# Performance work log

Measured on AMD Instinct MI355X. Metric: run time of the kernel, lower is better.

## Reference

```python
import jax, jax.numpy as jnp
import numpy as np
from jax import lax

C = 256      # in_c == out_c == dim
NH = 8       # num_heads
K = 7        # depthwise pos-enc kernel
H1 = 512     # int(mlp_ratio * in_c) = 2.0 * 256
B, Hs, Ws = 2, 48, 48


def setup_inputs() -> dict:
    key = jax.random.key(0)
    ks = jax.random.split(key, 8)
    w = lambda k, shape: jax.random.normal(k, shape, jnp.float32) * 0.02
    return {
        "x": jax.random.normal(ks[0], (B, C, Hs, Ws), jnp.float32),
        # 1x1 convs stored as [out, in] (BN folded into weight+bias)
        "qk_w": w(ks[1], (2 * C, C)), "qk_b": jnp.zeros((2 * C,), jnp.float32),
        "v_w": w(ks[2], (C, C)),       "v_b": jnp.zeros((C,), jnp.float32),
        # depthwise positional encoding conv [C,1,K,K]
        "pe_w": w(ks[3], (C, 1, K, K)), "pe_b": jnp.zeros((C,), jnp.float32),
        "proj_w": w(ks[4], (C, C)),    "proj_b": jnp.zeros((C,), jnp.float32),
        # conv FFN: 1x1 (SiLU) -> 1x1 (no act)
        "fc1_w": w(ks[5], (H1, C)),    "fc1_b": jnp.zeros((H1,), jnp.float32),
        "fc2_w": w(ks[6], (C, H1)),    "fc2_b": jnp.zeros((C,), jnp.float32),
    }


def _c1(x, w, b):
    # 1x1 conv == per-pixel matmul
    return jnp.einsum('bchw,oc->bohw', x, w) + b[None, :, None, None]


def reference(x, qk_w, qk_b, v_w, v_b, pe_w, pe_b, proj_w, proj_b,
              fc1_w, fc1_b, fc2_w, fc2_b):
    Bb, Cc, Hh, Ww = x.shape
    hd = Cc // NH                 # head_dim = 32
    N = Hh * Ww
    scale = hd ** -0.5

    # ---- AttentionV2 ----
    qk = _c1(x, qk_w, qk_b).reshape(Bb, NH, 2 * hd, N)
    q, k = qk[:, :, :hd], qk[:, :, hd:]
    v_full = _c1(x, v_w, v_b)                      # [B,C,H,W]
    pe = lax.conv_general_dilated(
        v_full, pe_w, (1, 1), 'SAME', feature_group_count=Cc,
        dimension_numbers=('NCHW', 'OIHW', 'NCHW')) + pe_b[None, :, None, None]
    v = v_full.reshape(Bb, NH, hd, N)

    # attn = q^T @ k * scale ; softmax over keys
    attn = jax.nn.softmax(jnp.einsum('bhdn,bhdm->bhnm', q, k) * scale, axis=-1)
    o = jnp.einsum('bhdm,bhnm->bhdn', v, attn).reshape(Bb, Cc, Hh, Ww)
    attn_out = _c1(o + pe, proj_w, proj_b)

    # ---- block residuals + conv FFN (add=True) ----
    x1 = x + attn_out
    h = jax.nn.silu(_c1(x1, fc1_w, fc1_b))         # Conv(in_c, hidden, 1, 1) with SiLU
    return x1 + _c1(h, fc2_w, fc2_b)               # Conv(hidden, out_c, 1, act=False)
```

## Files before the change

kernel.cpp:

```cpp
#include <hip/hip_runtime.h>
#include <hip/hip_bf16.h>

#define NCH 256
#define NHD 8
#define HD 32
#define NPIX 2304
#define H1DIM 512

typedef __attribute__((ext_vector_type(8))) __bf16 bf16x8;
typedef __attribute__((ext_vector_type(4))) float f32x4;

__global__ __launch_bounds__(256) void wcast_k(
    const float* __restrict__ w0, const float* __restrict__ w1,
    const float* __restrict__ w2, const float* __restrict__ w3,
    const float* __restrict__ w4, __bf16* __restrict__ dst) {
    int i = blockIdx.x * 256 + threadIdx.x;
    const float* src; int off;
    if (i < 32768)      { src = w0; off = i; }
    else if (i < 49152) { src = w1; off = i - 32768; }
    else if (i < 65536) { src = w2; off = i - 49152; }
    else if (i < 98304) { src = w3; off = i - 65536; }
    else                { src = w4; off = i - 98304; }
    float4 v = ((const float4*)src)[off];
    union { __bf16 h[4]; uint2 u; } pk;
    pk.h[0] = (__bf16)v.x; pk.h[1] = (__bf16)v.y;
    pk.h[2] = (__bf16)v.z; pk.h[3] = (__bf16)v.w;
    ((uint2*)dst)[i] = pk.u;
}

__global__ __launch_bounds__(256) void nchw2nhwc_k(const float* __restrict__ s1,
                                                   __bf16* __restrict__ dst) {
    const int tid = threadIdx.x;
    const int n0 = blockIdx.x * 64;
    const int c0 = blockIdx.y * 64;
    const int b = blockIdx.z;
    __shared__ float tile[64][65];
    const size_t sb = ((size_t)b * NCH + c0) * NPIX + n0;
#pragma unroll
    for (int i = 0; i < 16; ++i) {
        int idx = tid + i * 256;
        int r = idx >> 6, c = idx & 63;
        tile[r][c] = s1[sb + (size_t)r * NPIX + c];
    }
    __syncthreads();
#pragma unroll
    for (int i = 0; i < 8; ++i) {
        int idx = tid + i * 256;
        int nn = idx >> 5, cp = (idx & 31) * 2;
        union { __bf16 h[2]; unsigned u; } pk;
        pk.h[0] = (__bf16)tile[cp][nn];
        pk.h[1] = (__bf16)tile[cp + 1][nn];
        *(unsigned*)&dst[((size_t)b * NPIX + n0 + nn) * NCH + c0 + cp] = pk.u;
    }
}

template <int IC, int OC, int MODE>
__global__ __launch_bounds__(64) void convmm_k(
    const __bf16* __restrict__ A, const __bf16* __restrict__ W,
    const float* __restrict__ bias, const float* __restrict__ resid,
    float* __restrict__ out_f, __bf16* __restrict__ out_b,
    __bf16* __restrict__ out_b2) {
    const int lane = threadIdx.x;
    const int l16 = lane & 15, quad = lane >> 4;
    const int m0 = blockIdx.x * 16;
    const int oc0 = blockIdx.y * 16;
    const int b = blockIdx.z;

    const __bf16* aptr = A + ((size_t)b * NPIX + m0 + l16) * IC + quad * 8;
    const __bf16* bptr = W + (size_t)(oc0 + l16) * IC + quad * 8;

    f32x4 acc = {0.f, 0.f, 0.f, 0.f};
#pragma unroll 8
    for (int k = 0; k < IC; k += 32) {
        bf16x8 af = *(const bf16x8*)(aptr + k);
        bf16x8 bf = *(const bf16x8*)(bptr + k);
        acc = __builtin_amdgcn_mfma_f32_16x16x32_bf16(af, bf, acc, 0, 0, 0);
    }

    const int oc = oc0 + l16;
    const int mb = m0 + quad * 4;
    const float bb = bias[oc];

    if constexpr (MODE == 0) {
        const int h = oc0 >> 6;
        const int bh = b * NHD + h;
        const int dd = (oc0 & 16) + l16;
        if ((oc0 & 32) == 0) {
            const float qs = 0.17677669529663689f * 1.4426950408889634f;
#pragma unroll
            for (int r = 0; r < 4; ++r)
                out_b[((size_t)bh * NPIX + mb + r) * 32 + dd] = (__bf16)((acc[r] + bb) * qs);
        } else {
            __bf16* kp = out_b2 + ((size_t)(bh * 144 + (m0 >> 4)) * 64 + (dd >> 3) * 16 + quad * 4) * 8 + (dd & 7);
#pragma unroll
            for (int r = 0; r < 4; ++r) kp[r * 8] = (__bf16)(acc[r] + bb);
        }
    } else if constexpr (MODE == 1) {
        const int h = oc0 >> 5;
        const int bh = b * NHD + h;
        const int half = (oc0 >> 4) & 1;
        const size_t fb = ((size_t)b * OC + oc) * NPIX + mb;
        float4 vf_; float* vp = &vf_.x;
        union { __bf16 hh[4]; uint2 u; } pk;
#pragma unroll
        for (int r = 0; r < 4; ++r) {
            float v = acc[r] + bb;
            vp[r] = v; pk.hh[r] = (__bf16)v;
        }
        *(float4*)&out_f[fb] = vf_;
        *(uint2*)&out_b[((size_t)(bh * 144 + (m0 >> 4)) * 64 + lane) * 8 + half * 4] = pk.u;
    } else if constexpr (MODE == 2) {
        const size_t fb = ((size_t)b * OC + oc) * NPIX + mb;
        float4 xr = *(const float4*)&resid[fb];
        const float* xp = &xr.x;
        float4 vf_; float* vp = &vf_.x;
#pragma unroll
        for (int r = 0; r < 4; ++r) {
            float v = acc[r] + bb + xp[r];
            vp[r] = v;
            out_b[((size_t)b * NPIX + mb + r) * OC + oc] = (__bf16)v;
        }
        *(float4*)&out_f[fb] = vf_;
    } else if constexpr (MODE == 3) {
#pragma unroll
        for (int r = 0; r < 4; ++r) {
            float v = acc[r] + bb;
            v = v / (1.f + __expf(-v));
            out_b[((size_t)b * NPIX + mb + r) * OC + oc] = (__bf16)v;
        }
    } else {
        const size_t fb = ((size_t)b * OC + oc) * NPIX + mb;
        float4 xr = *(const float4*)&resid[fb];
        const float* xp = &xr.x;
        float4 vf_; float* vp = &vf_.x;
#pragma unroll
        for (int r = 0; r < 4; ++r) vp[r] = acc[r] + bb + xp[r];
        *(float4*)&out_f[fb] = vf_;
    }
}

__global__ __launch_bounds__(256) void dwconv_k(const float* __restrict__ vb,
                                                const float* __restrict__ pw,
                                                const float* __restrict__ pb,
                                                float* __restrict__ pe) {
    const int c = blockIdx.x, b = blockIdx.y, tid = threadIdx.x;
    __shared__ float plane[NPIX];
    __shared__ float wk[49];
    const size_t base = ((size_t)b * NCH + c) * NPIX;
    for (int i = tid; i < NPIX; i += 256) plane[i] = vb[base + i];
    if (tid < 49) wk[tid] = pw[c * 49 + tid];
    float bb = pb[c];
    __syncthreads();
    for (int p = tid; p < NPIX; p += 256) {
        int y = p / 48, x = p - y * 48;
        float s = bb;
#pragma unroll
        for (int ky = 0; ky < 7; ++ky) {
            int yy = y + ky - 3;
            if ((unsigned)yy < 48u) {
#pragma unroll
                for (int kx = 0; kx < 7; ++kx) {
                    int xx = x + kx - 3;
                    if ((unsigned)xx < 48u) s += wk[ky * 7 + kx] * plane[yy * 48 + xx];
                }
            }
        }
        pe[base + p] = s;
    }
}

__global__ __launch_bounds__(256) void attn_mfma4_k(const __bf16* __restrict__ Qb,
                                                    const __bf16* __restrict__ Kf,
                                                    const __bf16* __restrict__ Vf,
                                                    float* __restrict__ opart,
                                                    float* __restrict__ lpart) {
    const int tid = threadIdx.x;
    const int wave = tid >> 6, lane = tid & 63;
    const int l16 = lane & 15, quad = lane >> 4;
    const int nb = blockIdx.x * 128;
    const int h = blockIdx.y;
    const int b = blockIdx.z >> 2, ks = blockIdx.z & 3;
    const int bh = b * NHD + h;
    const int qb = nb + wave * 32;

    bf16x8 b_q0 = *(const bf16x8*)(Qb + ((size_t)bh * NPIX + qb + l16) * 32 + quad * 8);
    bf16x8 b_q1 = *(const bf16x8*)(Qb + ((size_t)bh * NPIX + qb + 16 + l16) * 32 + quad * 8);

    const __bf16* kf = Kf + ((size_t)(bh * 144 + ks * 36) * 64 + lane) * 8;
    const __bf16* vf = Vf + ((size_t)(bh * 144 + ks * 36) * 64 + lane) * 8;

    f32x4 o00 = {0.f,0.f,0.f,0.f}, o01 = {0.f,0.f,0.f,0.f};
    f32x4 o10 = {0.f,0.f,0.f,0.f}, o11 = {0.f,0.f,0.f,0.f};
    f32x4 l0 = {0.f,0.f,0.f,0.f}, l1 = {0.f,0.f,0.f,0.f};

#pragma unroll 3
    for (int t = 0; t < 36; ++t) {
        bf16x8 a_k = *(const bf16x8*)(kf + (size_t)t * 512);
        bf16x8 va  = *(const bf16x8*)(vf + (size_t)t * 512);
        f32x4 z = {0.f, 0.f, 0.f, 0.f};
        f32x4 s0 = __builtin_amdgcn_mfma_f32_16x16x32_bf16(a_k, b_q0, z, 0, 0, 0);
        f32x4 s1 = __builtin_amdgcn_mfma_f32_16x16x32_bf16(a_k, b_q1, z, 0, 0, 0);
        f32x4 p0, p1;
#pragma unroll
        for (int r = 0; r < 4; ++r) {
            p0[r] = __builtin_amdgcn_exp2f(s0[r]);
            p1[r] = __builtin_amdgcn_exp2f(s1[r]);
        }
        l0 += p0; l1 += p1;
        bf16x8 b0lo = {}, b0hi = {}, b1lo = {}, b1hi = {};
#pragma unroll
        for (int r = 0; r < 4; ++r) {
            __bf16 c0 = (__bf16)p0[r], c1 = (__bf16)p1[r];
            b0lo[r] = c0; b0hi[4 + r] = c0;
            b1lo[r] = c1; b1hi[4 + r] = c1;
        }
        o00 = __builtin_amdgcn_mfma_f32_16x16x32_bf16(va, b0lo, o00, 0, 0, 0);
        o01 = __builtin_amdgcn_mfma_f32_16x16x32_bf16(va, b0hi, o01, 0, 0, 0);
        o10 = __builtin_amdgcn_mfma_f32_16x16x32_bf16(va, b1lo, o10, 0, 0, 0);
        o11 = __builtin_amdgcn_mfma_f32_16x16x32_bf16(va, b1hi, o11, 0, 0, 0);
    }

    float ls0 = l0[0] + l0[1] + l0[2] + l0[3];
    ls0 += __shfl_xor(ls0, 16); ls0 += __shfl_xor(ls0, 32);
    float ls1 = l1[0] + l1[1] + l1[2] + l1[3];
    ls1 += __shfl_xor(ls1, 16); ls1 += __shfl_xor(ls1, 32);

    float* op = opart + (size_t)(ks * 16 + bh) * 32 * NPIX;
    const int n0 = qb + l16, n1 = qb + 16 + l16;
#pragma unroll
    for (int r = 0; r < 4; ++r) {
        op[(size_t)(quad * 4 + r) * NPIX + n0]      = o00[r];
        op[(size_t)(16 + quad * 4 + r) * NPIX + n0] = o01[r];
        op[(size_t)(quad * 4 + r) * NPIX + n1]      = o10[r];
        op[(size_t)(16 + quad * 4 + r) * NPIX + n1] = o11[r];
    }
    if (quad == 0) {
        lpart[(size_t)(ks * 16 + bh) * NPIX + n0] = ls0;
        lpart[(size_t)(ks * 16 + bh) * NPIX + n1] = ls1;
    }
}

__global__ __launch_bounds__(256) void merge2_k(const float* __restrict__ opart,
                                                const float* __restrict__ lpart,
                                                const float* __restrict__ pe,
                                                __bf16* __restrict__ opb) {
    const int tid = threadIdx.x;
    const int n0 = blockIdx.x * 64;
    const int h = blockIdx.y, b = blockIdx.z;
    const int bh = b * NHD + h;

    __shared__ float tinv[64];
    __shared__ float tile[64][33];

    if (tid < 64) {
        const int n = n0 + tid;
        float l = 0.f;
#pragma unroll
        for (int s = 0; s < 4; ++s) l += lpart[(size_t)(s * 16 + bh) * NPIX + n];
        tinv[tid] = 1.f / l;
    }
    __syncthreads();

#pragma unroll
    for (int pass = 0; pass < 8; ++pass) {
        const int idx = pass * 256 + tid;
        const int d = idx >> 6, c = idx & 63;
        float v = 0.f;
#pragma unroll
        for (int s = 0; s < 4; ++s)
            v += opart[((size_t)(s * 16 + bh) * 32 + d) * NPIX + n0 + c];
        v = v * tinv[c] + pe[((size_t)(b * NCH + h * HD + d)) * NPIX + n0 + c];
        tile[c][d] = v;
    }
    __syncthreads();

    const int n = tid >> 2, j = tid & 3;
    union { __bf16 hh[8]; uint4 u; } pk;
#pragma unroll
    for (int e = 0; e < 8; ++e) pk.hh[e] = (__bf16)tile[n][j * 8 + e];
    *(uint4*)&opb[((size_t)(b * NPIX + n0 + n)) * NCH + h * HD + j * 8] = pk.u;
}

extern "C" void kernel_launch(void* const* d_in, const int* in_sizes, int n_in,
                              void* d_out, int out_size, void* d_ws, size_t ws_size,
                              hipStream_t stream) {
    const float* x    = (const float*)d_in[0];
    const float* qk_w = (const float*)d_in[1];
    const float* qk_b = (const float*)d_in[2];
    const float* v_w  = (const float*)d_in[3];
    const float* v_b  = (const float*)d_in[4];
    const float* pe_w = (const float*)d_in[5];
    const float* pe_b = (const float*)d_in[6];
    const float* pj_w = (const float*)d_in[7];
    const float* pj_b = (const float*)d_in[8];
    const float* f1_w = (const float*)d_in[9];
    const float* f1_b = (const float*)d_in[10];
    const float* f2_w = (const float*)d_in[11];
    const float* f2_b = (const float*)d_in[12];
    float* out = (float*)d_out;

    const int B = 2;
    const size_t plane = (size_t)NCH * NPIX;
    const size_t bp = (size_t)B * plane;

    float* v_bu  = (float*)d_ws;
    float* pe_bu = v_bu + bp;
    float* x1_f  = pe_bu + bp;
    float* opart = x1_f + bp;
    float* lpart = opart + 4 * bp;
    __bf16* Xb   = (__bf16*)(lpart + 147456);
    __bf16* opb  = Xb + bp;
    __bf16* x1b  = opb + bp;
    __bf16* hb   = x1b + bp;
    __bf16* Qb   = hb + 2 * bp;
    __bf16* Kf   = Qb + bp;
    __bf16* Vf   = Kf + bp;
    __bf16* Wall = Vf + bp;
    __bf16* Wq = Wall;
    __bf16* Wv = Wall + 131072;
    __bf16* Wp = Wall + 196608;
    __bf16* W1 = Wall + 262144;
    __bf16* W2 = Wall + 393216;

    wcast_k<<<512, 256, 0, stream>>>(qk_w, v_w, pj_w, f1_w, f2_w, Wall);
    nchw2nhwc_k<<<dim3(NPIX / 64, 4, B), 256, 0, stream>>>(x, Xb);
    convmm_k<256, 512, 0><<<dim3(NPIX / 16, 32, B), 64, 0, stream>>>(
        Xb, Wq, qk_b, nullptr, nullptr, Qb, Kf);
    convmm_k<256, 256, 1><<<dim3(NPIX / 16, 16, B), 64, 0, stream>>>(
        Xb, Wv, v_b, nullptr, v_bu, Vf, nullptr);
    dwconv_k<<<dim3(NCH, B), 256, 0, stream>>>(v_bu, pe_w, pe_b, pe_bu);
    attn_mfma4_k<<<dim3(NPIX / 128, NHD, B * 4), 256, 0, stream>>>(Qb, Kf, Vf, opart, lpart);
    merge2_k<<<dim3(NPIX / 64, NHD, B), 256, 0, stream>>>(opart, lpart, pe_bu, opb);
    convmm_k<256, 256, 2><<<dim3(NPIX / 16, 16, B), 64, 0, stream>>>(
        opb, Wp, pj_b, x, x1_f, x1b, nullptr);
    convmm_k<256, 512, 3><<<dim3(NPIX / 16, 32, B), 64, 0, stream>>>(
        x1b, W1, f1_b, nullptr, nullptr, hb, nullptr);
    convmm_k<512, 256, 4><<<dim3(NPIX / 16, 16, B), 64, 0, stream>>>(
        hb, W2, f2_b, x1_f, out, nullptr, nullptr);
}
```

Baseline: 219.9 us.

## Fuse prep kernels, merge QK/V projections, drop attention split-K and merge pass

Combines the weight cast and NCHW-to-NHWC transpose into one launch, fuses the QK and V 1x1 projections into a single kernel, and removes the 4-way key split in attention so each wave normalizes and adds the positional encoding directly, eliminating the fp32 partial buffers and the merge kernel. The conv matmuls now pack four waves per block. Fewer launches and less intermediate traffic are the aim, but attention now runs 1152 single-wave blocks each iterating over all 144 key tiles, which reduces parallelism and lengthens the serial loop. Output stores become scattered 2-byte writes.

```diff
diff --git a/kernel.cpp b/kernel.cpp
--- a/kernel.cpp
+++ b/kernel.cpp
@@ -10,59 +10,122 @@
 typedef __attribute__((ext_vector_type(8))) __bf16 bf16x8;
 typedef __attribute__((ext_vector_type(4))) float f32x4;
 
-__global__ __launch_bounds__(256) void wcast_k(
+__global__ __launch_bounds__(256) void prep_k(
+    const float* __restrict__ x,
     const float* __restrict__ w0, const float* __restrict__ w1,
     const float* __restrict__ w2, const float* __restrict__ w3,
-    const float* __restrict__ w4, __bf16* __restrict__ dst) {
-    int i = blockIdx.x * 256 + threadIdx.x;
-    const float* src; int off;
-    if (i < 32768)      { src = w0; off = i; }
-    else if (i < 49152) { src = w1; off = i - 32768; }
-    else if (i < 65536) { src = w2; off = i - 49152; }
-    else if (i < 98304) { src = w3; off = i - 65536; }
-    else                { src = w4; off = i - 98304; }
-    float4 v = ((const float4*)src)[off];
-    union { __bf16 h[4]; uint2 u; } pk;
-    pk.h[0] = (__bf16)v.x; pk.h[1] = (__bf16)v.y;
-    pk.h[2] = (__bf16)v.z; pk.h[3] = (__bf16)v.w;
-    ((uint2*)dst)[i] = pk.u;
-}
-
-__global__ __launch_bounds__(256) void nchw2nhwc_k(const float* __restrict__ s1,
-                                                   __bf16* __restrict__ dst) {
+    const float* __restrict__ w4,
+    __bf16* __restrict__ Xb, __bf16* __restrict__ Wall) {
     const int tid = threadIdx.x;
-    const int n0 = blockIdx.x * 64;
-    const int c0 = blockIdx.y * 64;
+    if (blockIdx.x < 288) {
+        const int t = blockIdx.x;
+        const int b = t / 144, r0 = t % 144;
+        const int c0 = (r0 / 36) * 64, n0 = (r0 % 36) * 64;
+        __shared__ float tile[64][65];
+        const size_t sb = ((size_t)b * NCH + c0) * NPIX + n0;
+#pragma unroll
+        for (int i = 0; i < 16; ++i) {
+            int idx = tid + i * 256;
+            int rr = idx >> 6, cc = idx & 63;
+            tile[rr][cc] = x[sb + (size_t)rr * NPIX + cc];
+        }
+        __syncthreads();
+#pragma unroll
+        for (int i = 0; i < 8; ++i) {
+            int idx = tid + i * 256;
+            int nn = idx >> 5, cp = (idx & 31) * 2;
+            union { __bf16 h[2]; unsigned u; } pk;
+            pk.h[0] = (__bf16)tile[cp][nn];
+            pk.h[1] = (__bf16)tile[cp + 1][nn];
+            *(unsigned*)&Xb[((size_t)b * NPIX + n0 + nn) * NCH + c0 + cp] = pk.u;
+        }
+    } else {
+        int i = (blockIdx.x - 288) * 256 + tid;
+        const float* src; int off;
+        if (i < 32768)      { src = w0; off = i; }
+        else if (i < 49152) { src = w1; off = i - 32768; }
+        else if (i < 65536) { src = w2; off = i - 49152; }
+        else if (i < 98304) { src = w3; off = i - 65536; }
+        else                { src = w4; off = i - 98304; }
+        float4 v = ((const float4*)src)[off];
+        union { __bf16 h[4]; uint2 u; } pk;
+        pk.h[0] = (__bf16)v.x; pk.h[1] = (__bf16)v.y;
+        pk.h[2] = (__bf16)v.z; pk.h[3] = (__bf16)v.w;
+        ((uint2*)Wall)[i] = pk.u;
+    }
+}
+
+__global__ __launch_bounds__(256) void qkv_k(
+    const __bf16* __restrict__ A, const __bf16* __restrict__ Wq,
+    const __bf16* __restrict__ Wv, const float* __restrict__ qk_b,
+    const float* __restrict__ v_b, __bf16* __restrict__ Qb,
+    __bf16* __restrict__ Kf, float* __restrict__ v_bu,
+    __bf16* __restrict__ Vf) {
+    const int tid = threadIdx.x;
+    const int wave = tid >> 6, lane = tid & 63;
+    const int l16 = lane & 15, quad = lane >> 4;
+    const int m0 = blockIdx.x * 64 + wave * 16;
     const int b = blockIdx.z;
-    __shared__ float tile[64][65];
-    const size_t sb = ((size_t)b * NCH + c0) * NPIX + n0;
-#pragma unroll
-    for (int i = 0; i < 16; ++i) {
-        int idx = tid + i * 256;
-        int r = idx >> 6, c = idx & 63;
-        tile[r][c] = s1[sb + (size_t)r * NPIX + c];
-    }
-    __syncthreads();
-#pragma unroll
-    for (int i = 0; i < 8; ++i) {
-        int idx = tid + i * 256;
-        int nn = idx >> 5, cp = (idx & 31) * 2;
-        union { __bf16 h[2]; unsigned u; } pk;
-        pk.h[0] = (__bf16)tile[cp][nn];
-        pk.h[1] = (__bf16)tile[cp + 1][nn];
-        *(unsigned*)&dst[((size_t)b * NPIX + n0 + nn) * NCH + c0 + cp] = pk.u;
+    const bool isv = blockIdx.y >= 32;
+    const int oc0 = (isv ? (blockIdx.y - 32) : blockIdx.y) * 16;
+    const __bf16* W = isv ? Wv : Wq;
+
+    const __bf16* aptr = A + ((size_t)b * NPIX + m0 + l16) * NCH + quad * 8;
+    const __bf16* bptr = W + (size_t)(oc0 + l16) * NCH + quad * 8;
+
+    f32x4 acc = {0.f, 0.f, 0.f, 0.f};
+#pragma unroll 8
+    for (int k = 0; k < NCH; k += 32) {
+        bf16x8 af = *(const bf16x8*)(aptr + k);
+        bf16x8 bf = *(const bf16x8*)(bptr + k);
+        acc = __builtin_amdgcn_mfma_f32_16x16x32_bf16(af, bf, acc, 0, 0, 0);
+    }
+
+    const int oc = oc0 + l16;
+    const int mb = m0 + quad * 4;
+
+    if (!isv) {
+        const float bb = qk_b[oc];
+        const int h = oc0 >> 6;
+        const int bh = b * NHD + h;
+        const int dd = (oc0 & 16) + l16;
+        if ((oc0 & 32) == 0) {
+            const float qs = 0.17677669529663689f * 1.4426950408889634f;
+#pragma unroll
+            for (int r = 0; r < 4; ++r)
+                Qb[((size_t)bh * NPIX + mb + r) * 32 + dd] = (__bf16)((acc[r] + bb) * qs);
+        } else {
+            __bf16* kp = Kf + ((size_t)(bh * 144 + (m0 >> 4)) * 64 + (dd >> 3) * 16 + quad * 4) * 8 + (dd & 7);
+#pragma unroll
+            for (int r = 0; r < 4; ++r) kp[r * 8] = (__bf16)(acc[r] + bb);
+        }
+    } else {
+        const float bb = v_b[oc];
+        const int h = oc0 >> 5;
+        const int bh = b * NHD + h;
+        const int half = (oc0 >> 4) & 1;
+        const size_t fb = ((size_t)b * NCH + oc) * NPIX + mb;
+        float4 vf_; float* vp = &vf_.x;
+        union { __bf16 hh[4]; uint2 u; } pk;
+#pragma unroll
+        for (int r = 0; r < 4; ++r) {
+            float v = acc[r] + bb;
+            vp[r] = v; pk.hh[r] = (__bf16)v;
+        }
+        *(float4*)&v_bu[fb] = vf_;
+        *(uint2*)&Vf[((size_t)(bh * 144 + (m0 >> 4)) * 64 + lane) * 8 + half * 4] = pk.u;
     }
 }
 
 template <int IC, int OC, int MODE>
-__global__ __launch_bounds__(64) void convmm_k(
+__global__ __launch_bounds__(256) void convmm_k(
     const __bf16* __restrict__ A, const __bf16* __restrict__ W,
     const float* __restrict__ bias, const float* __restrict__ resid,
-    float* __restrict__ out_f, __bf16* __restrict__ out_b,
-    __bf16* __restrict__ out_b2) {
-    const int lane = threadIdx.x;
+    float* __restrict__ out_f, __bf16* __restrict__ out_b) {
+    const int tid = threadIdx.x;
+    const int wave = tid >> 6, lane = tid & 63;
     const int l16 = lane & 15, quad = lane >> 4;
-    const int m0 = blockIdx.x * 16;
+    const int m0 = blockIdx.x * 64 + wave * 16;
     const int oc0 = blockIdx.y * 16;
     const int b = blockIdx.z;
 
@@ -81,35 +144,7 @@
     const int mb = m0 + quad * 4;
     const float bb = bias[oc];
 
-    if constexpr (MODE == 0) {
-        const int h = oc0 >> 6;
-        const int bh = b * NHD + h;
-        const int dd = (oc0 & 16) + l16;
-        if ((oc0 & 32) == 0) {
-            const float qs = 0.17677669529663689f * 1.4426950408889634f;
-#pragma unroll
-            for (int r = 0; r < 4; ++r)
-                out_b[((size_t)bh * NPIX + mb + r) * 32 + dd] = (__bf16)((acc[r] + bb) * qs);
-        } else {
-            __bf16* kp = out_b2 + ((size_t)(bh * 144 + (m0 >> 4)) * 64 + (dd >> 3) * 16 + quad * 4) * 8 + (dd & 7);
-#pragma unroll
-            for (int r = 0; r < 4; ++r) kp[r * 8] = (__bf16)(acc[r] + bb);
-        }
-    } else if constexpr (MODE == 1) {
-        const int h = oc0 >> 5;
-        const int bh = b * NHD + h;
-        const int half = (oc0 >> 4) & 1;
-        const size_t fb = ((size_t)b * OC + oc) * NPIX + mb;
-        float4 vf_; float* vp = &vf_.x;
-        union { __bf16 hh[4]; uint2 u; } pk;
-#pragma unroll
-        for (int r = 0; r < 4; ++r) {
-            float v = acc[r] + bb;
-            vp[r] = v; pk.hh[r] = (__bf16)v;
-        }
-        *(float4*)&out_f[fb] = vf_;
-        *(uint2*)&out_b[((size_t)(bh * 144 + (m0 >> 4)) * 64 + lane) * 8 + half * 4] = pk.u;
-    } else if constexpr (MODE == 2) {
+    if constexpr (MODE == 2) {
         const size_t fb = ((size_t)b * OC + oc) * NPIX + mb;
         float4 xr = *(const float4*)&resid[fb];
         const float* xp = &xr.x;
@@ -169,32 +204,29 @@
     }
 }
 
-__global__ __launch_bounds__(256) void attn_mfma4_k(const __bf16* __restrict__ Qb,
-                                                    const __bf16* __restrict__ Kf,
-                                                    const __bf16* __restrict__ Vf,
-                                                    float* __restrict__ opart,
-                                                    float* __restrict__ lpart) {
-    const int tid = threadIdx.x;
-    const int wave = tid >> 6, lane = tid & 63;
+__global__ __launch_bounds__(64) void attn5_k(const __bf16* __restrict__ Qb,
+                                              const __bf16* __restrict__ Kf,
+                                              const __bf16* __restrict__ Vf,
+                                              const float* __restrict__ pe,
+                                              __bf16* __restrict__ opb) {
+    const int lane = threadIdx.x;
     const int l16 = lane & 15, quad = lane >> 4;
-    const int nb = blockIdx.x * 128;
-    const int h = blockIdx.y;
-    const int b = blockIdx.z >> 2, ks = blockIdx.z & 3;
+    const int qb = blockIdx.x * 32;
+    const int h = blockIdx.y, b = blockIdx.z;
     const int bh = b * NHD + h;
-    const int qb = nb + wave * 32;
 
     bf16x8 b_q0 = *(const bf16x8*)(Qb + ((size_t)bh * NPIX + qb + l16) * 32 + quad * 8);
     bf16x8 b_q1 = *(const bf16x8*)(Qb + ((size_t)bh * NPIX + qb + 16 + l16) * 32 + quad * 8);
 
-    const __bf16* kf = Kf + ((size_t)(bh * 144 + ks * 36) * 64 + lane) * 8;
-    const __bf16* vf = Vf + ((size_t)(bh * 144 + ks * 36) * 64 + lane) * 8;
+    const __bf16* kf = Kf + ((size_t)(bh * 144) * 64 + lane) * 8;
+    const __bf16* vf = Vf + ((size_t)(bh * 144) * 64 + lane) * 8;
 
     f32x4 o00 = {0.f,0.f,0.f,0.f}, o01 = {0.f,0.f,0.f,0.f};
     f32x4 o10 = {0.f,0.f,0.f,0.f}, o11 = {0.f,0.f,0.f,0.f};
     f32x4 l0 = {0.f,0.f,0.f,0.f}, l1 = {0.f,0.f,0.f,0.f};
 
-#pragma unroll 3
-    for (int t = 0; t < 36; ++t) {
+#pragma unroll 4
+    for (int t = 0; t < 144; ++t) {
         bf16x8 a_k = *(const bf16x8*)(kf + (size_t)t * 512);
         bf16x8 va  = *(const bf16x8*)(vf + (size_t)t * 512);
         f32x4 z = {0.f, 0.f, 0.f, 0.f};
@@ -224,61 +256,22 @@
     ls0 += __shfl_xor(ls0, 16); ls0 += __shfl_xor(ls0, 32);
     float ls1 = l1[0] + l1[1] + l1[2] + l1[3];
     ls1 += __shfl_xor(ls1, 16); ls1 += __shfl_xor(ls1, 32);
-
-    float* op = opart + (size_t)(ks * 16 + bh) * 32 * NPIX;
+    const float inv0 = 1.f / ls0, inv1 = 1.f / ls1;
+
     const int n0 = qb + l16, n1 = qb + 16 + l16;
+    const int ch0 = h * HD + quad * 4;
 #pragma unroll
     for (int r = 0; r < 4; ++r) {
-        op[(size_t)(quad * 4 + r) * NPIX + n0]      = o00[r];
-        op[(size_t)(16 + quad * 4 + r) * NPIX + n0] = o01[r];
-        op[(size_t)(quad * 4 + r) * NPIX + n1]      = o10[r];
-        op[(size_t)(16 + quad * 4 + r) * NPIX + n1] = o11[r];
-    }
-    if (quad == 0) {
-        lpart[(size_t)(ks * 16 + bh) * NPIX + n0] = ls0;
-        lpart[(size_t)(ks * 16 + bh) * NPIX + n1] = ls1;
-    }
-}
-
-__global__ __launch_bounds__(256) void merge2_k(const float* __restrict__ opart,
-                                                const float* __restrict__ lpart,
-                                                const float* __restrict__ pe,
-                                                __bf16* __restrict__ opb) {
-    const int tid = threadIdx.x;
-    const int n0 = blockIdx.x * 64;
-    const int h = blockIdx.y, b = blockIdx.z;
-    const int bh = b * NHD + h;
-
-    __shared__ float tinv[64];
-    __shared__ float tile[64][33];
-
-    if (tid < 64) {
-        const int n = n0 + tid;
-        float l = 0.f;
-#pragma unroll
-        for (int s = 0; s < 4; ++s) l += lpart[(size_t)(s * 16 + bh) * NPIX + n];
-        tinv[tid] = 1.f / l;
-    }
-    __syncthreads();
-
-#pragma unroll
-    for (int pass = 0; pass < 8; ++pass) {
-        const int idx = pass * 256 + tid;
-        const int d = idx >> 6, c = idx & 63;
-        float v = 0.f;
-#pragma unroll
-        for (int s = 0; s < 4; ++s)
-            v += opart[((size_t)(s * 16 + bh) * 32 + d) * NPIX + n0 + c];
-        v = v * tinv[c] + pe[((size_t)(b * NCH + h * HD + d)) * NPIX + n0 + c];
-        tile[c][d] = v;
-    }
-    __syncthreads();
-
-    const int n = tid >> 2, j = tid & 3;
-    union { __bf16 hh[8]; uint4 u; } pk;
-#pragma unroll
-    for (int e = 0; e < 8; ++e) pk.hh[e] = (__bf16)tile[n][j * 8 + e];
-    *(uint4*)&opb[((size_t)(b * NPIX + n0 + n)) * NCH + h * HD + j * 8] = pk.u;
+        const int ca = ch0 + r, cb = ch0 + 16 + r;
+        float pa0 = pe[((size_t)b * NCH + ca) * NPIX + n0];
+        float pb0 = pe[((size_t)b * NCH + cb) * NPIX + n0];
+        float pa1 = pe[((size_t)b * NCH + ca) * NPIX + n1];
+        float pb1 = pe[((size_t)b * NCH + cb) * NPIX + n1];
+        opb[((size_t)b * NPIX + n0) * NCH + ca] = (__bf16)(o00[r] * inv0 + pa0);
+        opb[((size_t)b * NPIX + n0) * NCH + cb] = (__bf16)(o01[r] * inv0 + pb0);
+        opb[((size_t)b * NPIX + n1) * NCH + ca] = (__bf16)(o10[r] * inv1 + pa1);
+        opb[((size_t)b * NPIX + n1) * NCH + cb] = (__bf16)(o11[r] * inv1 + pb1);
+    }
 }
 
 extern "C" void kernel_launch(void* const* d_in, const int* in_sizes, int n_in,
@@ -306,9 +299,7 @@
     float* v_bu  = (float*)d_ws;
     float* pe_bu = v_bu + bp;
     float* x1_f  = pe_bu + bp;
-    float* opart = x1_f + bp;
-    float* lpart = opart + 4 * bp;
-    __bf16* Xb   = (__bf16*)(lpart + 147456);
+    __bf16* Xb   = (__bf16*)(x1_f + bp);
     __bf16* opb  = Xb + bp;
     __bf16* x1b  = opb + bp;
     __bf16* hb   = x1b + bp;
@@ -322,19 +313,14 @@
     __bf16* W1 = Wall + 262144;
     __bf16* W2 = Wall + 393216;
 
-    wcast_k<<<512, 256, 0, stream>>>(qk_w, v_w, pj_w, f1_w, f2_w, Wall);
-    nchw2nhwc_k<<<dim3(NPIX / 64, 4, B), 256, 0, stream>>>(x, Xb);
-    convmm_k<256, 512, 0><<<dim3(NPIX / 16, 32, B), 64, 0, stream>>>(
-        Xb, Wq, qk_b, nullptr, nullptr, Qb, Kf);
-    convmm_k<256, 256, 1><<<dim3(NPIX / 16, 16, B), 64, 0, stream>>>(
-        Xb, Wv, v_b, nullptr, v_bu, Vf, nullptr);
+    prep_k<<<800, 256, 0, stream>>>(x, qk_w, v_w, pj_w, f1_w, f2_w, Xb, Wall);
+    qkv_k<<<dim3(36, 48, B), 256, 0, stream>>>(Xb, Wq, Wv, qk_b, v_b, Qb, Kf, v_bu, Vf);
     dwconv_k<<<dim3(NCH, B), 256, 0, stream>>>(v_bu, pe_w, pe_b, pe_bu);
-    attn_mfma4_k<<<dim3(NPIX / 128, NHD, B * 4), 256, 0, stream>>>(Qb, Kf, Vf, opart, lpart);
-    merge2_k<<<dim3(NPIX / 64, NHD, B), 256, 0, stream>>>(opart, lpart, pe_bu, opb);
-    convmm_k<256, 256, 2><<<dim3(NPIX / 16, 16, B), 64, 0, stream>>>(
-        opb, Wp, pj_b, x, x1_f, x1b, nullptr);
-    convmm_k<256, 512, 3><<<dim3(NPIX / 16, 32, B), 64, 0, stream>>>(
-        x1b, W1, f1_b, nullptr, nullptr, hb, nullptr);
-    convmm_k<512, 256, 4><<<dim3(NPIX / 16, 16, B), 64, 0, stream>>>(
-        hb, W2, f2_b, x1_f, out, nullptr, nullptr);
-}
+    attn5_k<<<dim3(NPIX / 32, NHD, B), 64, 0, stream>>>(Qb, Kf, Vf, pe_bu, opb);
+    convmm_k<256, 256, 2><<<dim3(36, 16, B), 256, 0, stream>>>(
+        opb, Wp, pj_b, x, x1_f, x1b);
+    convmm_k<256, 512, 3><<<dim3(36, 32, B), 256, 0, stream>>>(
+        x1b, W1, f1_b, nullptr, nullptr, hb);
+    convmm_k<512, 256, 4><<<dim3(36, 16, B), 256, 0, stream>>>(
+        hb, W2, f2_b, x1_f, out, nullptr);
+}
```

Result: slower. 237.8 us (+8.1%).
